# Performance work log

Measured on AMD Instinct MI355X. Metric: run time of the kernel, lower is better.

## Reference

```python
import jax, jax.numpy as jnp
import numpy as np

N = 50000
E = 1600000
IN_CH = 128
HID = 16
HEADS = 8
OUT_CH = 1
NEG_SLOPE = 0.2


def setup_inputs() -> dict:
    key = jax.random.key(0)
    ks = jax.random.split(key, 12)
    x = jax.random.normal(ks[0], (N, IN_CH), dtype=jnp.float32)
    edge_index = jax.random.randint(ks[1], (2, E), 0, N, dtype=jnp.int64)
    s1 = 1.0 / np.sqrt(IN_CH)
    s2 = 1.0 / np.sqrt(HEADS * HID)
    W1 = jax.random.normal(ks[2], (IN_CH, HEADS * HID), dtype=jnp.float32) * s1
    att_src1 = jax.random.normal(ks[3], (HEADS, HID), dtype=jnp.float32) * s1
    att_dst1 = jax.random.normal(ks[4], (HEADS, HID), dtype=jnp.float32) * s1
    b1 = jnp.zeros((HEADS * HID,), dtype=jnp.float32)
    W2 = jax.random.normal(ks[5], (HEADS * HID, OUT_CH), dtype=jnp.float32) * s2
    att_src2 = jax.random.normal(ks[6], (1, OUT_CH), dtype=jnp.float32) * s2
    att_dst2 = jax.random.normal(ks[7], (1, OUT_CH), dtype=jnp.float32) * s2
    b2 = jnp.zeros((OUT_CH,), dtype=jnp.float32)
    return {"x": x, "edge_index": edge_index,
            "W1": W1, "att_src1": att_src1, "att_dst1": att_dst1, "b1": b1,
            "W2": W2, "att_src2": att_src2, "att_dst2": att_dst2, "b2": b2}


def gat_conv(x, src, dst, W, att_src, att_dst, b, heads, concat):
    n = x.shape[0]
    h = (x @ W).reshape(n, heads, -1)               # [N, H, C]
    a_s = jnp.einsum('nhc,hc->nh', h, att_src)      # [N, H]
    a_d = jnp.einsum('nhc,hc->nh', h, att_dst)
    e = jax.nn.leaky_relu(a_s[src] + a_d[dst], NEG_SLOPE)  # [E, H]
    # segment softmax over incoming edges of each dst node
    emax = jax.ops.segment_max(e, dst, num_segments=n)
    p = jnp.exp(e - emax[dst])
    denom = jax.ops.segment_sum(p, dst, num_segments=n)
    alpha = p / (denom[dst] + 1e-16)                 # [E, H]
    msg = h[src] * alpha[:, :, None]                 # [E, H, C]
    out = jax.ops.segment_sum(msg, dst, num_segments=n)  # [N, H, C]
    if concat:
        out = out.reshape(n, -1)
    else:
        out = out.mean(axis=1)
    return out + b


def reference(x, edge_index, W1, att_src1, att_dst1, b1, W2, att_src2, att_dst2, b2):
    n = x.shape[0]
    loops = jnp.arange(n, dtype=edge_index.dtype)
    src = jnp.concatenate([edge_index[0], loops])    # PyG add_self_loops=True
    dst = jnp.concatenate([edge_index[1], loops])
    h = gat_conv(x, src, dst, W1, att_src1, att_dst1, b1, HEADS, True)
    h = jax.nn.elu(h)
    out = gat_conv(h, src, dst, W2, att_src2, att_dst2, b2, 1, False)
    return out
```

## Files before the change

kernel.cpp:

```cpp
#include <hip/hip_runtime.h>
#include <hip/hip_fp16.h>
#include <math.h>

#define N_NODES 50000
#define N_EDGES 1600000
#define NEG 0.2f

#define PB 256
#define CHUNK (N_EDGES / PB)
#define EPT 25
#define BSHIFT 4
#define NBUCK (N_NODES >> BSHIFT)
#define STRIDE 768
#define GEMMB ((N_NODES + 31) / 32)


__global__ __launch_bounds__(256) void scatter_gemm(const int* __restrict__ ei, int* __restrict__ bcnt,
                                                    int* __restrict__ temp,
                                                    const float* __restrict__ x, const float* __restrict__ W1,
                                                    const float* __restrict__ att_s, const float* __restrict__ att_d,
                                                    __half2* __restrict__ h1, float* __restrict__ as1,
                                                    float* __restrict__ ad1) {
    __shared__ union {
        float xs[128][36];
        int cur[NBUCK];
    } u;
    int t = threadIdx.x;
    if (blockIdx.x < PB) {
        int p = blockIdx.x;
        for (int i = t; i < NBUCK; i += 256) u.cur[i] = 0;
        __syncthreads();
        int e0 = p * CHUNK;
        int vc[EPT];
#pragma unroll
        for (int k = 0; k < EPT; ++k) {
            vc[k] = -1;
            int off = t + k * 256;
            if (off < CHUNK) {
                int e = e0 + off;
                int s = ei[e];
                int d = ei[N_EDGES + e];
                vc[k] = s | (d << 16);
                atomicAdd(&u.cur[d >> BSHIFT], 1);
            }
        }
        __syncthreads();
        for (int i = t; i < NBUCK; i += 256) {
            int h = u.cur[i];
            int c = i * STRIDE;
            if (h) c += atomicAdd(&bcnt[i], h);
            u.cur[i] = c;
        }
        __syncthreads();
#pragma unroll
        for (int k = 0; k < EPT; ++k) {
            int v = vc[k];
            if (v != -1) {
                unsigned d = (unsigned)v >> 16;
                int b = d >> BSHIFT;
                int pos = atomicAdd(&u.cur[b], 1);
                if (pos < (b + 1) * STRIDE)
                    temp[pos] = (v & 0xFFFF) | ((d & 15) << 16);
            }
        }
        return;
    }
    int n0 = (blockIdx.x - PB) * 32;
#pragma unroll
    for (int i = 0; i < 16; ++i) {
        int f = i * 256 + t;
        int r = f >> 7, c = f & 127;
        int gr = n0 + r;
        float v = (gr < N_NODES) ? x[(size_t)gr * 128 + c] : 0.f;
        u.xs[c][r] = v;
    }
    __syncthreads();
    int c0 = (t & 31) * 4;
    int r0 = (t >> 5) * 4;
    float acc[4][4];
#pragma unroll
    for (int i = 0; i < 4; ++i)
#pragma unroll
        for (int j = 0; j < 4; ++j) acc[i][j] = 0.f;
#pragma unroll 4
    for (int k = 0; k < 128; ++k) {
        float4 w = *(const float4*)(W1 + k * 128 + c0);
        float4 xr = *(const float4*)(&u.xs[k][r0]);
        float xv[4] = {xr.x, xr.y, xr.z, xr.w};
        float wv[4] = {w.x, w.y, w.z, w.w};
#pragma unroll
        for (int i = 0; i < 4; ++i)
#pragma unroll
            for (int j = 0; j < 4; ++j) acc[i][j] += xv[i] * wv[j];
    }
#pragma unroll
    for (int i = 0; i < 4; ++i) {
        int row = n0 + r0 + i;
        if (row < N_NODES) {
            __half2 p0 = __float22half2_rn(make_float2(acc[i][0], acc[i][1]));
            __half2 p1 = __float22half2_rn(make_float2(acc[i][2], acc[i][3]));
            h1[(size_t)row * 64 + (c0 >> 1)] = p0;
            h1[(size_t)row * 64 + (c0 >> 1) + 1] = p1;
        }
    }
    int head = (t & 31) >> 2;
    float ps[4], pd[4];
#pragma unroll
    for (int i = 0; i < 4; ++i) {
        float s = 0.f, d = 0.f;
#pragma unroll
        for (int j = 0; j < 4; ++j) {
            s += acc[i][j] * att_s[c0 + j];
            d += acc[i][j] * att_d[c0 + j];
        }
        ps[i] = s; pd[i] = d;
    }
#pragma unroll
    for (int i = 0; i < 4; ++i) {
        ps[i] += __shfl_xor(ps[i], 1, 64);
        ps[i] += __shfl_xor(ps[i], 2, 64);
        pd[i] += __shfl_xor(pd[i], 1, 64);
        pd[i] += __shfl_xor(pd[i], 2, 64);
    }
    if ((t & 3) == 0) {
#pragma unroll
        for (int i = 0; i < 4; ++i) {
            int row = n0 + r0 + i;
            if (row < N_NODES) {
                as1[row * 8 + head] = ps[i];
                ad1[row * 8 + head] = pd[i];
            }
        }
    }
}


__device__ __forceinline__ float lrelu(float v) { return fmaxf(v, NEG * v); }

__global__ __launch_bounds__(128) void agg1_kernel(const char* __restrict__ h1c, const char* __restrict__ as1c,
                                                   const float* __restrict__ ad1, const int* __restrict__ temp,
                                                   const int* __restrict__ bcnt, const float* __restrict__ b1,
                                                   const float* __restrict__ W2, float* __restrict__ h2out) {
    __shared__ int lsrc[STRIDE];
    __shared__ int cnt[16];
    __shared__ int cur[16];
    __shared__ int lrp[16];
    int b = blockIdx.x, t = threadIdx.x;
    int base = b * STRIDE;
    int nE = min(bcnt[b], STRIDE);
    if (t < 16) cnt[t] = 0;
    __syncthreads();
    for (int i = t; i < nE; i += 128)
        atomicAdd(&cnt[(unsigned)temp[base + i] >> 16], 1);
    __syncthreads();
    if (t < 16) {
        int v = cnt[t];
        int incl = v;
#pragma unroll
        for (int off = 1; off < 16; off <<= 1) {
            int u = __shfl_up(incl, off, 16);
            if (t >= off) incl += u;
        }
        int excl = incl - v;
        lrp[t] = excl;
        cur[t] = excl;
    }
    __syncthreads();
    for (int i = t; i < nE; i += 128) {
        int v = temp[base + i];
        int pos = atomicAdd(&cur[(unsigned)v >> 16], 1);
        lsrc[pos] = v & 0xFFFF;
    }
    __syncthreads();

    int lane = t & 63;
    int wave = t >> 6;
    int hB = lane >> 3;
    int hP = lane & 7;
    unsigned lane4 = (unsigned)lane << 2;
    unsigned hP4 = (unsigned)hP << 2;
    int bperm_base = hB << 2;
    int prod = lane >> 3;

    for (int kk = 0; kk < 8; ++kk) {
        int k = wave * 8 + kk;
        int n = b * 16 + k;

        float adP = ad1[n * 8 + hP];
        float adC = ad1[n * 8 + hB];
        float asC = *(const float*)(as1c + ((unsigned)n * 32u + ((unsigned)hB << 2)));
        float p_self = __expf(lrelu(asC + adC));
        __half2 hvs = *(const __half2*)(h1c + (((unsigned)n << 8) + lane4));
        float acc0 = p_self * __half2float(__low2half(hvs));
        float acc1 = p_self * __half2float(__high2half(hvs));
        float l = p_self;

        int jb = lrp[k];
        int deg = cnt[k];
        int j = 0;
        for (; j + 8 <= deg; j += 8) {
            int sP = lsrc[jb + j + prod];
            float aP = *(const float*)(as1c + (((unsigned)sP << 5) + hP4));
            float pP = __expf(lrelu(aP + adP));
            int pPi = __float_as_int(pP);
#pragma unroll
            for (int e = 0; e < 8; ++e) {
                int addr = bperm_base + e * 32;
                float p = __int_as_float(__builtin_amdgcn_ds_bpermute(addr, pPi));
                int s = __builtin_amdgcn_ds_bpermute(addr, sP);
                __half2 hv = *(const __half2*)(h1c + (((unsigned)s << 8) + lane4));
                acc0 += p * __half2float(__low2half(hv));
                acc1 += p * __half2float(__high2half(hv));
                l += p;
            }
        }
        if (j < deg) {
            int r = deg - j;
            int sP = 0;
            float pP = 0.f;
            if (j + prod < deg) {
                sP = lsrc[jb + j + prod];
                float aP = *(const float*)(as1c + (((unsigned)sP << 5) + hP4));
                pP = __expf(lrelu(aP + adP));
            }
            int pPi = __float_as_int(pP);
            for (int e = 0; e < r; ++e) {
                int addr = bperm_base + e * 32;
                float p = __int_as_float(__builtin_amdgcn_ds_bpermute(addr, pPi));
                int s = __builtin_amdgcn_ds_bpermute(addr, sP);
                __half2 hv = *(const __half2*)(h1c + (((unsigned)s << 8) + lane4));
                acc0 += p * __half2float(__low2half(hv));
                acc1 += p * __half2float(__high2half(hv));
                l += p;
            }
        }

        float inv = 1.f / (l + 1e-16f);
        int c0 = lane * 2;
        float y0 = acc0 * inv + b1[c0];
        float y1 = acc1 * inv + b1[c0 + 1];
        y0 = y0 > 0.f ? y0 : expm1f(y0);
        y1 = y1 > 0.f ? y1 : expm1f(y1);
        float part = y0 * W2[c0] + y1 * W2[c0 + 1];
#pragma unroll
        for (int off = 32; off; off >>= 1) part += __shfl_down(part, off, 64);
        if (lane == 0) h2out[n] = part;
    }
}


__global__ __launch_bounds__(128) void agg2_kernel(const float* __restrict__ h2, const int* __restrict__ temp,
                                                   const int* __restrict__ bcnt, const float* __restrict__ att_s2,
                                                   const float* __restrict__ att_d2, const float* __restrict__ b2,
                                                   float* __restrict__ out) {
    __shared__ int lsrc[STRIDE];
    __shared__ int cnt[16];
    __shared__ int cur[16];
    __shared__ int lrp[16];
    int b = blockIdx.x, t = threadIdx.x;
    int base = b * STRIDE;
    int nE = min(bcnt[b], STRIDE);
    if (t < 16) cnt[t] = 0;
    __syncthreads();
    for (int i = t; i < nE; i += 128)
        atomicAdd(&cnt[(unsigned)temp[base + i] >> 16], 1);
    __syncthreads();
    if (t < 16) {
        int v = cnt[t];
        int incl = v;
#pragma unroll
        for (int off = 1; off < 16; off <<= 1) {
            int u = __shfl_up(incl, off, 16);
            if (t >= off) incl += u;
        }
        int excl = incl - v;
        lrp[t] = excl;
        cur[t] = excl;
    }
    __syncthreads();
    for (int i = t; i < nE; i += 128) {
        int v = temp[base + i];
        int pos = atomicAdd(&cur[(unsigned)v >> 16], 1);
        lsrc[pos] = v & 0xFFFF;
    }
    __syncthreads();

    float asw = att_s2[0], adw = att_d2[0];
    int lane = t & 63;
    int wave = t >> 6;
    int sub = lane & 7;
    int k = wave * 8 + (lane >> 3);
    int n = b * 16 + k;
    float h2n = h2[n];
    float ad = h2n * adw;
    float acc = 0.f, l = 0.f;
    if (sub == 0) {
        float p = __expf(lrelu(h2n * asw + ad));
        acc = p * h2n;
        l = p;
    }
    int jb = lrp[k];
    int deg = cnt[k];
    for (int jj = sub; jj < deg; jj += 8) {
        int s = lsrc[jb + jj];
        float hs = h2[s];
        float p = __expf(lrelu(hs * asw + ad));
        acc += p * hs;
        l += p;
    }
#pragma unroll
    for (int off = 4; off; off >>= 1) {
        acc += __shfl_down(acc, off, 8);
        l += __shfl_down(l, off, 8);
    }
    if (sub == 0) out[n] = acc / (l + 1e-16f) + b2[0];
}


extern "C" void kernel_launch(void* const* d_in, const int* in_sizes, int n_in,
                              void* d_out, int out_size, void* d_ws, size_t ws_size,
                              hipStream_t stream) {
    const float* x = (const float*)d_in[0];
    const int* ei = (const int*)d_in[1];
    const float* W1 = (const float*)d_in[2];
    const float* att_s1 = (const float*)d_in[3];
    const float* att_d1 = (const float*)d_in[4];
    const float* b1 = (const float*)d_in[5];
    const float* W2 = (const float*)d_in[6];
    const float* att_s2 = (const float*)d_in[7];
    const float* att_d2 = (const float*)d_in[8];
    const float* b2 = (const float*)d_in[9];
    float* out = (float*)d_out;

    char* p = (char*)d_ws;
    auto alloc = [&](size_t bytes) {
        char* q = p;
        p += (bytes + 255) & ~(size_t)255;
        return q;
    };
    int* bcnt = (int*)alloc((size_t)NBUCK * 4);
    int* temp = (int*)alloc((size_t)NBUCK * STRIDE * 4);
    __half2* h1 = (__half2*)alloc((size_t)N_NODES * 128 * 2);
    float* as1 = (float*)alloc((size_t)N_NODES * 8 * 4);
    float* ad1 = (float*)alloc((size_t)N_NODES * 8 * 4);
    float* h2 = (float*)alloc((size_t)N_NODES * 4);

    hipMemsetAsync(bcnt, 0, (size_t)NBUCK * 4, stream);
    scatter_gemm<<<PB + GEMMB, 256, 0, stream>>>(ei, bcnt, temp,
                                                 x, W1, att_s1, att_d1, h1, as1, ad1);
    agg1_kernel<<<NBUCK, 128, 0, stream>>>((const char*)h1, (const char*)as1, ad1, temp, bcnt, b1, W2, h2);
    agg2_kernel<<<NBUCK, 128, 0, stream>>>(h2, temp, bcnt, att_s2, att_d2, b2, out);
}
```

Before: 214.6 us.

## Replace shared-memory bucket counting scatter with direct global atomics per edge

The edge bucketing phase previously used 256 large blocks, each counting edges into per-bucket shared-memory histograms before reserving global ranges and scattering. It now launches 3125 small blocks where each thread handles two edges and does a global atomicAdd on the bucket counter to get its slot. This removes the shared histogram passes, the block barriers and the 25-element register array, and it spreads the work across many more blocks. In exchange it issues one global atomic per edge instead of one per block-bucket pair, which adds contention on the bucket counters.

```diff
diff --git a/kernel.cpp b/kernel.cpp
--- a/kernel.cpp
+++ b/kernel.cpp
@@ -6,9 +6,8 @@
 #define N_EDGES 1600000
 #define NEG 0.2f
 
-#define PB 256
-#define CHUNK (N_EDGES / PB)
-#define EPT 25
+#define SB 3125
+#define SCHUNK 512
 #define BSHIFT 4
 #define NBUCK (N_NODES >> BSHIFT)
 #define STRIDE 768
@@ -21,58 +20,30 @@
                                                     const float* __restrict__ att_s, const float* __restrict__ att_d,
                                                     __half2* __restrict__ h1, float* __restrict__ as1,
                                                     float* __restrict__ ad1) {
-    __shared__ union {
-        float xs[128][36];
-        int cur[NBUCK];
-    } u;
+    __shared__ float xs[128][36];
     int t = threadIdx.x;
-    if (blockIdx.x < PB) {
-        int p = blockIdx.x;
-        for (int i = t; i < NBUCK; i += 256) u.cur[i] = 0;
-        __syncthreads();
-        int e0 = p * CHUNK;
-        int vc[EPT];
-#pragma unroll
-        for (int k = 0; k < EPT; ++k) {
-            vc[k] = -1;
-            int off = t + k * 256;
-            if (off < CHUNK) {
-                int e = e0 + off;
-                int s = ei[e];
-                int d = ei[N_EDGES + e];
-                vc[k] = s | (d << 16);
-                atomicAdd(&u.cur[d >> BSHIFT], 1);
-            }
-        }
-        __syncthreads();
-        for (int i = t; i < NBUCK; i += 256) {
-            int h = u.cur[i];
-            int c = i * STRIDE;
-            if (h) c += atomicAdd(&bcnt[i], h);
-            u.cur[i] = c;
-        }
-        __syncthreads();
-#pragma unroll
-        for (int k = 0; k < EPT; ++k) {
-            int v = vc[k];
-            if (v != -1) {
-                unsigned d = (unsigned)v >> 16;
-                int b = d >> BSHIFT;
-                int pos = atomicAdd(&u.cur[b], 1);
-                if (pos < (b + 1) * STRIDE)
-                    temp[pos] = (v & 0xFFFF) | ((d & 15) << 16);
-            }
+    if (blockIdx.x < SB) {
+        int e0 = blockIdx.x * SCHUNK;
+#pragma unroll
+        for (int k = 0; k < 2; ++k) {
+            int e = e0 + k * 256 + t;
+            int s = ei[e];
+            int d = ei[N_EDGES + e];
+            int bkt = d >> BSHIFT;
+            int pos = atomicAdd(&bcnt[bkt], 1);
+            if (pos < STRIDE)
+                temp[bkt * STRIDE + pos] = s | ((d & 15) << 16);
         }
         return;
     }
-    int n0 = (blockIdx.x - PB) * 32;
+    int n0 = (blockIdx.x - SB) * 32;
 #pragma unroll
     for (int i = 0; i < 16; ++i) {
         int f = i * 256 + t;
         int r = f >> 7, c = f & 127;
         int gr = n0 + r;
         float v = (gr < N_NODES) ? x[(size_t)gr * 128 + c] : 0.f;
-        u.xs[c][r] = v;
+        xs[c][r] = v;
     }
     __syncthreads();
     int c0 = (t & 31) * 4;
@@ -85,7 +56,7 @@
 #pragma unroll 4
     for (int k = 0; k < 128; ++k) {
         float4 w = *(const float4*)(W1 + k * 128 + c0);
-        float4 xr = *(const float4*)(&u.xs[k][r0]);
+        float4 xr = *(const float4*)(&xs[k][r0]);
         float xv[4] = {xr.x, xr.y, xr.z, xr.w};
         float wv[4] = {w.x, w.y, w.z, w.w};
 #pragma unroll
@@ -346,7 +317,7 @@
     float* h2 = (float*)alloc((size_t)N_NODES * 4);
 
     hipMemsetAsync(bcnt, 0, (size_t)NBUCK * 4, stream);
-    scatter_gemm<<<PB + GEMMB, 256, 0, stream>>>(ei, bcnt, temp,
+    scatter_gemm<<<SB + GEMMB, 256, 0, stream>>>(ei, bcnt, temp,
                                                  x, W1, att_s1, att_d1, h1, as1, ad1);
     agg1_kernel<<<NBUCK, 128, 0, stream>>>((const char*)h1, (const char*)as1, ad1, temp, bcnt, b1, W2, h2);
     agg2_kernel<<<NBUCK, 128, 0, stream>>>(h2, temp, bcnt, att_s2, att_d2, b2, out);
```

After: 342.9 us. +59.8%, slower.
